# Optimization experiments

Measured on AMD Instinct MI355X. Metric: run time of the kernel, lower is better.

Reference implementation:

```python
import jax, jax.numpy as jnp
import numpy as np
from jax import lax

C, NORI, NROT, K, PAD = 256, 8, 2, 3, 1
B, H, W = 16, 64, 64
EPS = 1e-5


def setup_inputs() -> dict:
    key = jax.random.key(0)
    k1, k2, k3 = jax.random.split(key, 3)
    x = jax.random.normal(k1, (B, C, H, W), dtype=jnp.float32)
    # rotate_arf() output: [nRot*C, nOri*C, K, K]
    weight_all = jax.random.normal(k2, (NROT * C, NORI * C, K, K), dtype=jnp.float32) * 0.02
    bias_all = jax.random.normal(k3, (NROT * C,), dtype=jnp.float32) * 0.02
    alpha = jnp.float32(1.0)
    gamma = jnp.ones((C,), dtype=jnp.float32)
    beta = jnp.zeros((C,), dtype=jnp.float32)
    return {"x": x, "weight_all": weight_all, "bias_all": bias_all,
            "alpha": alpha, "gamma": gamma, "beta": beta}


def _forward(x, weight_all, bias_all, alpha, gamma, beta):
    # Loop of nOri*nRot convs over the same x with different weight blocks,
    # all accumulated into one [B,C,H,W] tensor == single conv with summed blocks
    # (conv is linear in the weights): fused form of the original loop.
    W_eff = weight_all.reshape(NROT, C, NORI, C, K, K).sum(axis=(0, 2))  # [C, C, K, K]
    b_eff = bias_all.reshape(NROT, C).sum(axis=0) * NORI                 # [C]
    d_sum = lax.conv_general_dilated(
        x, W_eff, window_strides=(1, 1), padding=[(PAD, PAD), (PAD, PAD)],
        dimension_numbers=("NCHW", "OIHW", "NCHW"))
    d_sum = d_sum + b_eff[None, :, None, None]
    d_mean = d_sum / float(NORI * NROT)
    out = x + alpha * d_mean
    # BatchNorm2d, training mode: biased batch stats over (B, H, W)
    mean = out.mean(axis=(0, 2, 3))
    var = ((out - mean[None, :, None, None]) ** 2).mean(axis=(0, 2, 3))
    inv = lax.rsqrt(var + EPS)
    y = (out - mean[None, :, None, None]) * (gamma * inv)[None, :, None, None] \
        + beta[None, :, None, None]
    return y


def reference(x, weight_all, bias_all, alpha, gamma, beta):
    return _forward(x, weight_all, bias_all, alpha, gamma, beta)
```

## Files before the change

### kernel.cpp

```cpp
#include <hip/hip_runtime.h>
#include <stdint.h>

typedef __attribute__((__ext_vector_type__(8))) __bf16 bf16x8;
typedef __attribute__((__ext_vector_type__(4))) float  f32x4;

#define XT_OFF    0ul
#define WT_OFF    33554432ul
#define BEFF_OFF  34734080ul
#define ZERO_OFF  34737152ul
#define STATS_OFF 34737408ul

__device__ inline void gload_lds16(const void* g, void* l) {
  __builtin_amdgcn_global_load_lds((const __attribute__((address_space(1))) void*)g,
                                   (__attribute__((address_space(3))) void*)l,
                                   16, 0, 0);
}

__global__ void k_wred(const float* __restrict__ w, const float* __restrict__ bias,
                       const float* __restrict__ alpha_p, __bf16* __restrict__ Wt,
                       float* __restrict__ beff, float* __restrict__ zerob,
                       float* __restrict__ statsG) {
  const int co = blockIdx.x;
  const int ci = threadIdx.x;
  float a[9];
#pragma unroll
  for (int t = 0; t < 9; ++t) a[t] = 0.f;
#pragma unroll
  for (int r = 0; r < 2; ++r)
#pragma unroll
    for (int o = 0; o < 8; ++o) {
      const float* p = w + ((size_t)(r * 256 + co) * 2048 + (size_t)(o * 256 + ci)) * 9;
#pragma unroll
      for (int t = 0; t < 9; ++t) a[t] += p[t];
    }
  const float sc = alpha_p[0] * 0.0625f;
  const int s = ci >> 6, cis = ci & 63;
#pragma unroll
  for (int t = 0; t < 9; ++t)
    Wt[(size_t)(t * 4 + s) * 16384 + co * 64 + cis] = (__bf16)(a[t] * sc);
  if (ci == 0) beff[co] = (bias[co] + bias[256 + co]) * 8.0f * sc;
  if (blockIdx.x == 0) {
    statsG[ci] = 0.f; statsG[256 + ci] = 0.f;
    if (ci < 64) zerob[ci] = 0.f;
  }
}

__global__ void k_xpose(const float* __restrict__ x, __bf16* __restrict__ xT) {
  __shared__ __bf16 lds[64 * 258];
  int bh = blockIdx.x;
  int b = bh >> 6, h = bh & 63;
  int t = threadIdx.x;
  int w = t & 63, cg = t >> 6;
  const float* xb = x + ((size_t)b * 16384 + h) * 64;
#pragma unroll 4
  for (int cb = 0; cb < 256; cb += 4) {
    int ci = cb + cg;
    lds[w * 258 + ci] = (__bf16)xb[(size_t)ci * 4096 + w];
  }
  __syncthreads();
  const uint32_t* l32 = (const uint32_t*)lds;
  uint32_t* o32 = (uint32_t*)(xT + ((size_t)b * 64 + h) * 64 * 256);
  int c2 = t & 127, wg = t >> 7;
  for (int w0 = 0; w0 < 64; w0 += 2) {
    int ww = w0 + wg;
    o32[ww * 128 + c2] = l32[ww * 129 + c2];
  }
}

#define A_BYTES 51200
#define B_BYTES 32768

__global__ __launch_bounds__(512) void k_conv(
    const float* __restrict__ x, const __bf16* __restrict__ xT,
    const __bf16* __restrict__ Wt, const float* __restrict__ beff,
    const __bf16* __restrict__ zerob, float* __restrict__ out,
    float* __restrict__ statsG)
{
  __shared__ __align__(16) char lds[A_BYTES + 3 * B_BYTES];
  const int bb   = blockIdx.x >> 4;
  const int ho0  = (blockIdx.x & 15) << 2;
  const int tid  = threadIdx.x;
  const int lane = tid & 63;
  const int wid  = tid >> 6;
  const int wr   = wid >> 2;
  const int wc   = wid & 3;

  f32x4 acc[8][4];
#pragma unroll
  for (int i = 0; i < 8; ++i)
#pragma unroll
    for (int j = 0; j < 4; ++j)
#pragma unroll
      for (int r = 0; r < 4; ++r) acc[i][j][r] = 0.f;

  const char* zb = (const char*)zerob;

  int boff[4][2];
#pragma unroll
  for (int j = 0; j < 4; ++j)
#pragma unroll
    for (int kk = 0; kk < 2; ++kk) {
      const int co     = (wc << 6) + (j << 4) + (lane & 15);
      const int ci_off = (kk << 5) + ((lane >> 4) << 3);
      boff[j][kk] = ((co << 7) + (ci_off << 1)) ^ ((co & 7) << 4);
    }
  const int bl = lane >> 3;
  const int bsrcLane = (bl << 7) + (((lane & 7) ^ (bl & 7)) << 4);

  auto stageA = [&](int s) {
    const int ci0 = s << 6;
    for (int t = wid; t < 50; t += 8) {
      const int ch = (t << 3) + (lane >> 3);
      const int r  = ch / 66;
      const int c  = ch - r * 66;
      const int ir = ho0 - 1 + r;
      const int ic = c - 1;
      const int k  = (lane & 7) ^ (ch & 7);
      const char* src;
      if (ch < 396 && ir >= 0 && ir < 64 && ic >= 0 && ic < 64)
        src = (const char*)(xT + ((((size_t)bb << 6) + ir) * 64 + ic) * 256 + ci0 + (k << 3));
      else
        src = zb + (k << 4);
      gload_lds16(src, lds + (t << 10));
    }
  };

  auto stageB = [&](int ph) {
    char* buf = lds + A_BYTES + (ph % 3) * B_BYTES;
    const int tap = ph / 4 - (ph / 36) * 9;
    (void)tap;
    const int s2 = ph / 9, tp = ph - s2 * 9;
    const char* wsrc = (const char*)Wt + ((size_t)(tp * 4 + s2) << 15) + bsrcLane;
#pragma unroll
    for (int it = 0; it < 4; ++it) {
      const int t = wid + (it << 3);
      gload_lds16(wsrc + (t << 10), buf + (t << 10));
    }
  };

  stageA(0);
  stageB(0);
  stageB(1);
  asm volatile("s_waitcnt vmcnt(4)" ::: "memory");
  __builtin_amdgcn_s_barrier();

  int s = 0, tap = 0;
  for (int p = 0; p < 36; ++p) {
    if (p > 0) {
      if (p == 35) asm volatile("s_waitcnt vmcnt(0)" ::: "memory");
      else         asm volatile("s_waitcnt vmcnt(4)" ::: "memory");
      __builtin_amdgcn_s_barrier();
    }
    const bool bnd = (tap == 0) && (p > 0);
    if (bnd) stageA(s);
    if (p + 2 < 36) stageB(p + 2);
    if (bnd) asm volatile("s_waitcnt vmcnt(4)" ::: "memory");

    const int dh = (tap >= 6) ? 2 : (tap >= 3 ? 1 : 0);
    const int dw = tap - dh * 3;
    const char* Bb = lds + A_BYTES + (p % 3) * B_BYTES;
    __builtin_amdgcn_s_setprio(1);
#pragma unroll
    for (int kk = 0; kk < 2; ++kk) {
      const int ci_off = (kk << 5) + ((lane >> 4) << 3);
      bf16x8 av[8];
#pragma unroll
      for (int i = 0; i < 8; ++i) {
        const int pos = ((wr << 1) + (i >> 2) + dh) * 66 + ((i & 3) << 4) + (lane & 15) + dw;
        const int off = ((pos << 7) + (ci_off << 1)) ^ ((pos & 7) << 4);
        av[i] = *(const bf16x8*)(lds + off);
      }
#pragma unroll
      for (int j = 0; j < 4; ++j) {
        const bf16x8 bv = *(const bf16x8*)(Bb + boff[j][kk]);
#pragma unroll
        for (int i = 0; i < 8; ++i)
          acc[i][j] = __builtin_amdgcn_mfma_f32_16x16x32_bf16(av[i], bv, acc[i][j], 0, 0, 0);
      }
    }
    __builtin_amdgcn_s_setprio(0);

    if (++tap == 9) { tap = 0; ++s; }
  }

  __syncthreads();
  float* sw    = (float*)lds + wid * 2064;
  float* lstat = (float*)(lds + 131072);
  if (tid < 512) lstat[tid] = 0.f;
  __syncthreads();

  const int cl = lane & 15, ch4 = (lane >> 4) << 2;
  const int cc2 = lane >> 2, q = lane & 3;
#pragma unroll
  for (int j = 0; j < 4; ++j) {
    asm volatile("s_waitcnt lgkmcnt(0)" ::: "memory");
#pragma unroll
    for (int i = 0; i < 8; ++i)
#pragma unroll
      for (int r = 0; r < 4; ++r)
        sw[cl * 129 + (i << 4) + ch4 + r] = acc[i][j][r];
    asm volatile("s_waitcnt lgkmcnt(0)" ::: "memory");
    for (int cc = 0; cc < 16; ++cc) {
      const int co = (wc << 6) + (j << 4) + cc;
      const float be = beff[co];
#pragma unroll
      for (int half = 0; half < 2; ++half) {
        const float conv = sw[cc * 129 + (half << 6) + lane];
        const int ho = ho0 + (wr << 1) + half;
        const size_t oi = ((((size_t)bb << 8) + (size_t)co) << 12) + (ho << 6) + lane;
        const float v = x[oi] + conv + be;
        out[oi] = v;
        sw[cc * 129 + (half << 6) + lane] = v;
      }
    }
    asm volatile("s_waitcnt lgkmcnt(0)" ::: "memory");
    float r1 = 0.f, r2 = 0.f;
#pragma unroll
    for (int k = 0; k < 32; ++k) {
      const float vv = sw[cc2 * 129 + (q << 5) + k];
      r1 += vv; r2 += vv * vv;
    }
    r1 += __shfl_xor(r1, 1); r2 += __shfl_xor(r2, 1);
    r1 += __shfl_xor(r1, 2); r2 += __shfl_xor(r2, 2);
    if (q == 0) {
      const int co = (wc << 6) + (j << 4) + cc2;
      atomicAdd(&lstat[co], r1);
      atomicAdd(&lstat[256 + co], r2);
    }
    asm volatile("s_waitcnt lgkmcnt(0)" ::: "memory");
  }
  __syncthreads();
  if (tid < 512) atomicAdd(&statsG[tid], lstat[tid]);
}

__global__ void k_apply(float* __restrict__ out, const float* __restrict__ statsG,
                        const float* __restrict__ gamma, const float* __restrict__ beta) {
  size_t i = (size_t)blockIdx.x * 256 + threadIdx.x;
  int co = (int)((i >> 10) & 255);
  const float mean = statsG[co] * (1.f / 65536.f);
  const float var  = statsG[256 + co] * (1.f / 65536.f) - mean * mean;
  const float inv  = rsqrtf(var + 1e-5f);
  const float sc   = gamma[co] * inv;
  const float sh   = beta[co] - mean * sc;
  float4* p = (float4*)out;
  float4 v = p[i];
  v.x = v.x * sc + sh; v.y = v.y * sc + sh; v.z = v.z * sc + sh; v.w = v.w * sc + sh;
  p[i] = v;
}

extern "C" void kernel_launch(void* const* d_in, const int* in_sizes, int n_in,
                              void* d_out, int out_size, void* d_ws, size_t ws_size,
                              hipStream_t stream) {
  const float* x     = (const float*)d_in[0];
  const float* wall  = (const float*)d_in[1];
  const float* bias  = (const float*)d_in[2];
  const float* alpha = (const float*)d_in[3];
  const float* gamma = (const float*)d_in[4];
  const float* beta  = (const float*)d_in[5];
  float* out = (float*)d_out;

  char* ws = (char*)d_ws;
  __bf16* xT     = (__bf16*)(ws + XT_OFF);
  __bf16* Wt     = (__bf16*)(ws + WT_OFF);
  float*  beff   = (float*)(ws + BEFF_OFF);
  float*  zerob  = (float*)(ws + ZERO_OFF);
  float*  statsG = (float*)(ws + STATS_OFF);

  k_wred<<<256, 256, 0, stream>>>(wall, bias, alpha, Wt, beff, zerob, statsG);
  k_xpose<<<1024, 256, 0, stream>>>(x, xT);
  k_conv<<<256, 512, 0, stream>>>(x, xT, Wt, beff, (const __bf16*)zerob, out, statsG);
  k_apply<<<16384, 256, 0, stream>>>(out, statsG, gamma, beta);
}
```

Baseline: 130.9 us.

## Restructure conv MFMA loop to interleave LDS fragment loads with MFMA groups

Reorganizes the inner tap loop of the implicit-GEMM conv so all B fragments and the first two A fragment sets are loaded up front. The remaining A fragments are then loaded between MFMA groups, with setprio toggling around each group. LDS addresses are precomputed once per tap as base offsets plus constant strides, and the ring-buffer index is tracked incrementally instead of using p%3. The epilogue drops the explicit lgkmcnt waits in favour of one barrier per j iteration. The aim is to hide LDS read latency behind MFMA work and cut address arithmetic, at the cost of more live VGPRs for the fragment arrays.

```diff
diff --git a/kernel.cpp b/kernel.cpp
--- a/kernel.cpp
+++ b/kernel.cpp
@@ -69,6 +69,16 @@
 
 #define A_BYTES 51200
 #define B_BYTES 32768
+
+#define MFMA16(RH, AV, BV)                                                      \
+  _Pragma("unroll")                                                             \
+  for (int j = 0; j < 4; ++j) {                                                 \
+    _Pragma("unroll")                                                           \
+    for (int q = 0; q < 4; ++q)                                                 \
+      acc[(RH) * 4 + q][j] =                                                    \
+        __builtin_amdgcn_mfma_f32_16x16x32_bf16(AV[q], BV[j],                   \
+                                                acc[(RH) * 4 + q][j], 0, 0, 0); \
+  }
 
 __global__ __launch_bounds__(512) void k_conv(
     const float* __restrict__ x, const __bf16* __restrict__ xT,
@@ -84,6 +94,7 @@
   const int wid  = tid >> 6;
   const int wr   = wid >> 2;
   const int wc   = wid & 3;
+  const int l15  = lane & 15;
 
   f32x4 acc[8][4];
 #pragma unroll
@@ -95,15 +106,9 @@
 
   const char* zb = (const char*)zerob;
 
-  int boff[4][2];
-#pragma unroll
-  for (int j = 0; j < 4; ++j)
-#pragma unroll
-    for (int kk = 0; kk < 2; ++kk) {
-      const int co     = (wc << 6) + (j << 4) + (lane & 15);
-      const int ci_off = (kk << 5) + ((lane >> 4) << 3);
-      boff[j][kk] = ((co << 7) + (ci_off << 1)) ^ ((co & 7) << 4);
-    }
+  const int co0 = (wc << 6) + l15;
+  const int bb0 = (((co0 << 7) + ((lane >> 4) << 4)) ^ ((co0 & 7) << 4));
+  const int bb1 = (((co0 << 7) + ((lane >> 4) << 4) + 64) ^ ((co0 & 7) << 4));
   const int bl = lane >> 3;
   const int bsrcLane = (bl << 7) + (((lane & 7) ^ (bl & 7)) << 4);
 
@@ -125,10 +130,8 @@
     }
   };
 
-  auto stageB = [&](int ph) {
-    char* buf = lds + A_BYTES + (ph % 3) * B_BYTES;
-    const int tap = ph / 4 - (ph / 36) * 9;
-    (void)tap;
+  auto stageB = [&](int ph, int bi) {
+    char* buf = lds + A_BYTES + bi * B_BYTES;
     const int s2 = ph / 9, tp = ph - s2 * 9;
     const char* wsrc = (const char*)Wt + ((size_t)(tp * 4 + s2) << 15) + bsrcLane;
 #pragma unroll
@@ -139,12 +142,12 @@
   };
 
   stageA(0);
-  stageB(0);
-  stageB(1);
+  stageB(0, 0);
+  stageB(1, 1);
   asm volatile("s_waitcnt vmcnt(4)" ::: "memory");
   __builtin_amdgcn_s_barrier();
 
-  int s = 0, tap = 0;
+  int s = 0, tap = 0, bcur = 0;
   for (int p = 0; p < 36; ++p) {
     if (p > 0) {
       if (p == 35) asm volatile("s_waitcnt vmcnt(0)" ::: "memory");
@@ -153,34 +156,50 @@
     }
     const bool bnd = (tap == 0) && (p > 0);
     if (bnd) stageA(s);
-    if (p + 2 < 36) stageB(p + 2);
+    if (p + 2 < 36) {
+      int bnx = bcur + 2; if (bnx >= 3) bnx -= 3;
+      stageB(p + 2, bnx);
+    }
     if (bnd) asm volatile("s_waitcnt vmcnt(4)" ::: "memory");
 
     const int dh = (tap >= 6) ? 2 : (tap >= 3 ? 1 : 0);
     const int dw = tap - dh * 3;
-    const char* Bb = lds + A_BYTES + (p % 3) * B_BYTES;
+    const char* Bb = lds + A_BYTES + bcur * B_BYTES;
+    const int pr0  = ((wr << 1) + dh) * 66 + l15 + dw;
+    const int pr1  = pr0 + 66;
+    const int cib  = (lane >> 4) << 4;
+    const int ab00 = (((pr0 << 7) + cib) ^ ((pr0 & 7) << 4));
+    const int ab01 = (((pr1 << 7) + cib) ^ ((pr1 & 7) << 4));
+    const int ab10 = (((pr0 << 7) + cib + 64) ^ ((pr0 & 7) << 4));
+    const int ab11 = (((pr1 << 7) + cib + 64) ^ ((pr1 & 7) << 4));
+
+    bf16x8 bv0[4], bv1[4], a0[4], a1[4], a2[4], a3[4];
+#pragma unroll
+    for (int j = 0; j < 4; ++j) bv0[j] = *(const bf16x8*)(Bb + bb0 + (j << 11));
+#pragma unroll
+    for (int j = 0; j < 4; ++j) bv1[j] = *(const bf16x8*)(Bb + bb1 + (j << 11));
+#pragma unroll
+    for (int q = 0; q < 4; ++q) a0[q] = *(const bf16x8*)(lds + ab00 + (q << 11));
+#pragma unroll
+    for (int q = 0; q < 4; ++q) a1[q] = *(const bf16x8*)(lds + ab01 + (q << 11));
+
     __builtin_amdgcn_s_setprio(1);
-#pragma unroll
-    for (int kk = 0; kk < 2; ++kk) {
-      const int ci_off = (kk << 5) + ((lane >> 4) << 3);
-      bf16x8 av[8];
-#pragma unroll
-      for (int i = 0; i < 8; ++i) {
-        const int pos = ((wr << 1) + (i >> 2) + dh) * 66 + ((i & 3) << 4) + (lane & 15) + dw;
-        const int off = ((pos << 7) + (ci_off << 1)) ^ ((pos & 7) << 4);
-        av[i] = *(const bf16x8*)(lds + off);
-      }
-#pragma unroll
-      for (int j = 0; j < 4; ++j) {
-        const bf16x8 bv = *(const bf16x8*)(Bb + boff[j][kk]);
-#pragma unroll
-        for (int i = 0; i < 8; ++i)
-          acc[i][j] = __builtin_amdgcn_mfma_f32_16x16x32_bf16(av[i], bv, acc[i][j], 0, 0, 0);
-      }
-    }
+    MFMA16(0, a0, bv0);
     __builtin_amdgcn_s_setprio(0);
+#pragma unroll
+    for (int q = 0; q < 4; ++q) a2[q] = *(const bf16x8*)(lds + ab10 + (q << 11));
+    __builtin_amdgcn_s_setprio(1);
+    MFMA16(1, a1, bv0);
+    __builtin_amdgcn_s_setprio(0);
+#pragma unroll
+    for (int q = 0; q < 4; ++q) a3[q] = *(const bf16x8*)(lds + ab11 + (q << 11));
+    __builtin_amdgcn_s_setprio(1);
+    MFMA16(0, a2, bv1);
+    MFMA16(1, a3, bv1);
+    __builtin_amdgcn_s_setprio(0);
 
     if (++tap == 9) { tap = 0; ++s; }
+    if (++bcur == 3) bcur = 0;
   }
 
   __syncthreads();
@@ -190,16 +209,14 @@
   __syncthreads();
 
   const int cl = lane & 15, ch4 = (lane >> 4) << 2;
-  const int cc2 = lane >> 2, q = lane & 3;
+  const int cc2 = lane >> 2, q2 = lane & 3;
 #pragma unroll
   for (int j = 0; j < 4; ++j) {
-    asm volatile("s_waitcnt lgkmcnt(0)" ::: "memory");
 #pragma unroll
     for (int i = 0; i < 8; ++i)
 #pragma unroll
       for (int r = 0; r < 4; ++r)
         sw[cl * 129 + (i << 4) + ch4 + r] = acc[i][j][r];
-    asm volatile("s_waitcnt lgkmcnt(0)" ::: "memory");
     for (int cc = 0; cc < 16; ++cc) {
       const int co = (wc << 6) + (j << 4) + cc;
       const float be = beff[co];
@@ -213,23 +230,21 @@
         sw[cc * 129 + (half << 6) + lane] = v;
       }
     }
-    asm volatile("s_waitcnt lgkmcnt(0)" ::: "memory");
     float r1 = 0.f, r2 = 0.f;
 #pragma unroll
     for (int k = 0; k < 32; ++k) {
-      const float vv = sw[cc2 * 129 + (q << 5) + k];
+      const float vv = sw[cc2 * 129 + (q2 << 5) + k];
       r1 += vv; r2 += vv * vv;
     }
     r1 += __shfl_xor(r1, 1); r2 += __shfl_xor(r2, 1);
     r1 += __shfl_xor(r1, 2); r2 += __shfl_xor(r2, 2);
-    if (q == 0) {
+    if (q2 == 0) {
       const int co = (wc << 6) + (j << 4) + cc2;
       atomicAdd(&lstat[co], r1);
       atomicAdd(&lstat[256 + co], r2);
     }
-    asm volatile("s_waitcnt lgkmcnt(0)" ::: "memory");
-  }
-  __syncthreads();
+    __syncthreads();
+  }
   if (tid < 512) atomicAdd(&statsG[tid], lstat[tid]);
 }
 
```

Measured after the change: 129.7 us. No clear change (-0.9%).
